# Optimization experiments

Hardware: AMD Instinct MI355X
Metric: run time of the kernel (lower is better)

The kernel has to match this reference:

```python
import jax, jax.numpy as jnp
import numpy as np

Q_PTS = jnp.array([0.0, 0.25, 0.5, 0.75, 1.0], dtype=jnp.float32)
LN_EPS = 1e-5


def _lower_median(s):
    # torch.median returns the LOWER of the two middle values for even n
    return s[..., (s.shape[-1] - 1) // 2]


def _quantile_sorted(s, q):
    # torch.quantile default 'linear' interpolation, computed on pre-sorted s
    n = s.shape[-1]
    idx = q * (n - 1)
    lo = jnp.floor(idx).astype(jnp.int32)
    hi = jnp.ceil(idx).astype(jnp.int32)
    frac = (idx - lo).astype(s.dtype)
    return jnp.take(s, lo, axis=-1) * (1.0 - frac) + jnp.take(s, hi, axis=-1) * frac


def _robust_stats(flat):
    # flat: [L-1, B, N] -> [L-1, B, 7]  (median, MAD, 5 quantiles)
    s = jnp.sort(flat, axis=-1)
    med = _lower_median(s)[..., None]
    mad = _lower_median(jnp.sort(jnp.abs(flat - med), axis=-1))[..., None]
    q = _quantile_sorted(s, Q_PTS)
    return jnp.concatenate([med, mad, q], axis=-1)


def _layer_norm(x, eps=LN_EPS):
    mu = x.mean(-1, keepdims=True)
    var = ((x - mu) ** 2).mean(-1, keepdims=True)
    return (x - mu) * jax.lax.rsqrt(var + eps)


def _forward(ws, bs, fc1_w, fc1_b, ln_w, ln_b, gate_w, gate_b, fco_w, fco_b, scale):
    Lm1, B = ws.shape[0], ws.shape[1]
    w_flat = ws.reshape(Lm1, B, -1)
    b_flat = bs.reshape(Lm1, B, -1)
    w_feats = _robust_stats(w_flat)            # [L-1, B, 7]
    b_feats = _robust_stats(b_flat)            # [L-1, B, 7]
    g_mean = w_flat.mean(-1, keepdims=True)    # [L-1, B, 1]
    g_mad = jnp.zeros_like(g_mean)             # MAD over a size-1 axis is exactly 0
    combined = jnp.concatenate([w_feats, b_feats, g_mean, g_mad], axis=-1)  # [L-1, B, 16]
    x = _layer_norm(combined)                  # F.layer_norm without affine
    # ResidualMLP (vectorized over the layer axis l)
    h = jnp.einsum('lbi,lhi->lbh', x, fc1_w) + fc1_b[:, None, :]
    h = _layer_norm(h) * ln_w[:, None, :] + ln_b[:, None, :]
    h = jax.nn.gelu(h, approximate=False)      # nn.GELU() default = exact erf
    gate = jax.nn.sigmoid(jnp.einsum('lbh,lgh->lbg', h, gate_w) + gate_b[:, None, :])
    raw = jnp.einsum('lbg,log->lbo', h * gate, fco_w) + fco_b[:, None, :]
    return jnp.sin(raw) * scale[:, None, None] + 1.0   # [L-1, B, out_dim]


def setup_inputs() -> dict:
    key = jax.random.key(0)
    ks = jax.random.split(key, 8)
    Lm1, B, D, H, F_IN = 3, 64, 512, 64, 16
    return {
        'ws': jax.random.normal(ks[0], (Lm1, B, D, D), jnp.float32) * 0.05,
        'bs': jax.random.normal(ks[1], (Lm1, B, D), jnp.float32) * 0.05,
        'w_last': jax.random.normal(ks[2], (B, D, D), jnp.float32) * 0.05,
        'b_last': jax.random.normal(ks[3], (B, D), jnp.float32) * 0.05,
        'fc1_w': jax.random.normal(ks[4], (Lm1, H, F_IN), jnp.float32) * 0.2,
        'fc1_b': jnp.zeros((Lm1, H), jnp.float32),
        'ln_w': jnp.ones((Lm1, H), jnp.float32),
        'ln_b': jnp.zeros((Lm1, H), jnp.float32),
        'gate_w': jax.random.normal(ks[5], (Lm1, H, H), jnp.float32) * 0.15,
        'gate_b': jnp.zeros((Lm1, H), jnp.float32),
        'fco_w': jax.random.normal(ks[6], (Lm1, D, H), jnp.float32) * 0.1,
        'fco_b': jnp.zeros((Lm1, D), jnp.float32),
        'scale': jnp.full((Lm1,), 0.1, jnp.float32),
    }


def reference(ws, bs, w_last, b_last, fc1_w, fc1_b, ln_w, ln_b, gate_w, gate_b, fco_w, fco_b, scale):
    # w_last / b_last correspond to wsfeat[L-1]: received by forward but never used
    # (loop breaks at i == L-1), matching the torch module exactly.
    return _forward(ws, bs, fc1_w, fc1_b, ln_w, ln_b, gate_w, gate_b, fco_w, fco_b, scale)
```

## Files before the change

kernel.cpp:

```cpp
#include <hip/hip_runtime.h>
#include <cstdint>

#define LM1   3
#define BDIM  64
#define NROW  (LM1 * BDIM)
#define DDIM  512
#define NW    (DDIM * DDIM)
#define NW4   (NW / 4)
#define WT    1024
#define CAP   30720

__device__ __forceinline__ uint32_t mono(float x) {
    uint32_t u = __float_as_uint(x);
    return (u & 0x80000000u) ? ~u : (u | 0x80000000u);
}
__device__ __forceinline__ float unmono(uint32_t u) {
    uint32_t v = (u & 0x80000000u) ? (u & 0x7FFFFFFFu) : ~u;
    return __uint_as_float(v);
}

__device__ void block_select(const uint32_t* hist, int nb, uint32_t rank,
                             uint32_t* sbuf, uint32_t* out_bin, uint32_t* out_rem,
                             int tid) {
    const int NT = WT;
    int per = (nb + NT - 1) / NT;
    int base = tid * per;
    uint32_t s = 0;
    for (int i = 0; i < per; ++i) {
        int idx = base + i;
        if (idx < nb) s += hist[idx];
    }
    sbuf[tid] = s;
    __syncthreads();
    uint32_t run = s;
    for (int off = 1; off < NT; off <<= 1) {
        uint32_t add = (tid >= off) ? sbuf[tid - off] : 0u;
        __syncthreads();
        run += add;
        sbuf[tid] = run;
        __syncthreads();
    }
    uint32_t incl = run;
    uint32_t excl = incl - s;
    if (rank >= excl && rank < incl) {
        uint32_t rem = rank - excl;
        for (int i = 0; i < per; ++i) {
            int idx = base + i;
            if (idx >= nb) break;
            uint32_t c = hist[idx];
            if (rem < c) { *out_bin = (uint32_t)idx; *out_rem = rem; break; }
            rem -= c;
        }
    }
    __syncthreads();
}

__device__ uint32_t refine_lds(const uint32_t* cbuf, uint32_t off, uint32_t cnt,
                               uint32_t rem, uint32_t b1,
                               uint32_t* hist2, uint32_t* sbuf,
                               uint32_t* stmp, int tid) {
    for (int i = tid; i < 2048; i += WT) hist2[i] = 0;
    __syncthreads();
    for (uint32_t i = tid; i < cnt; i += WT) {
        uint32_t u = cbuf[off + i];
        atomicAdd(&hist2[(u >> 9) & 2047u], 1u);
    }
    __syncthreads();
    block_select(hist2, 2048, rem, sbuf, &stmp[0], &stmp[1], tid);
    uint32_t b2 = stmp[0], r2 = stmp[1];
    __syncthreads();
    for (int i = tid; i < 512; i += WT) hist2[i] = 0;
    __syncthreads();
    for (uint32_t i = tid; i < cnt; i += WT) {
        uint32_t u = cbuf[off + i];
        if (((u >> 9) & 2047u) == b2) atomicAdd(&hist2[u & 511u], 1u);
    }
    __syncthreads();
    block_select(hist2, 512, r2, sbuf, &stmp[0], &stmp[1], tid);
    uint32_t b3 = stmp[0];
    __syncthreads();
    return (b1 << 20) | (b2 << 9) | b3;
}

__device__ uint32_t refine_global(const float4* p4, uint32_t phase, float med, int mode,
                                  uint32_t b1, uint32_t rem,
                                  uint32_t* hist2, uint32_t* sbuf,
                                  uint32_t* stmp, int tid) {
    for (int i = tid; i < 2048; i += WT) hist2[i] = 0;
    __syncthreads();
    for (int it = 0; it < 64; ++it) {
        float4 v = p4[(tid + it * WT + phase) & (NW4 - 1)];
        float xs[4] = {v.x, v.y, v.z, v.w};
        #pragma unroll
        for (int c = 0; c < 4; ++c) {
            uint32_t u = mode ? __float_as_uint(fabsf(xs[c] - med)) : mono(xs[c]);
            if ((u >> 20) == b1) atomicAdd(&hist2[(u >> 9) & 2047u], 1u);
        }
    }
    __syncthreads();
    block_select(hist2, 2048, rem, sbuf, &stmp[0], &stmp[1], tid);
    uint32_t b2 = stmp[0], r2 = stmp[1];
    __syncthreads();
    for (int i = tid; i < 512; i += WT) hist2[i] = 0;
    __syncthreads();
    for (int it = 0; it < 64; ++it) {
        float4 v = p4[(tid + it * WT + phase) & (NW4 - 1)];
        float xs[4] = {v.x, v.y, v.z, v.w};
        #pragma unroll
        for (int c = 0; c < 4; ++c) {
            uint32_t u = mode ? __float_as_uint(fabsf(xs[c] - med)) : mono(xs[c]);
            if ((u >> 20) == b1 && ((u >> 9) & 2047u) == b2)
                atomicAdd(&hist2[u & 511u], 1u);
        }
    }
    __syncthreads();
    block_select(hist2, 512, r2, sbuf, &stmp[0], &stmp[1], tid);
    uint32_t b3 = stmp[0];
    __syncthreads();
    return (b1 << 20) | (b2 << 9) | b3;
}

__global__ __launch_bounds__(WT) void wstats_kernel(const float* __restrict__ wsrc,
                                                    float* __restrict__ feat) {
    const int row = blockIdx.x;
    const int tid = threadIdx.x;
    const float4* __restrict__ p4 = (const float4*)(wsrc + (size_t)row * NW);
    const uint32_t phase = ((uint32_t)row * 341u) & (NW4 - 1);

    __shared__ uint32_t lds[4096 + CAP + 2048 + 1024];
    uint32_t* hist  = lds;
    uint32_t* cbuf  = lds + 4096;
    uint32_t* hist2 = lds + 4096 + CAP;
    uint32_t* sbuf  = lds + 4096 + CAP + 2048;
    __shared__ uint32_t s_bin[8], s_rem[8];
    __shared__ uint32_t s_dbin[8], s_cnt[8], s_off[9], s_cur[8], s_rdj[8];
    __shared__ uint32_t s_nd, s_T, stmp[2], s_sv[8];
    __shared__ float s_med;

    for (int i = tid; i < 4096; i += WT) hist[i] = 0;
    __syncthreads();
    float sum = 0.f;
    for (int it = 0; it < 64; it += 8) {
        float4 a[8];
        #pragma unroll
        for (int j = 0; j < 8; ++j)
            a[j] = p4[(tid + (it + j) * WT + phase) & (NW4 - 1)];
        #pragma unroll
        for (int j = 0; j < 8; ++j) {
            float xs[4] = {a[j].x, a[j].y, a[j].z, a[j].w};
            #pragma unroll
            for (int c = 0; c < 4; ++c) {
                sum += xs[c];
                uint32_t u = mono(xs[c]);
                atomicAdd(&hist[u >> 20], 1u);
            }
        }
    }
    {
        float* sbf = (float*)sbuf;
        sbf[tid] = sum; __syncthreads();
        for (int o = WT / 2; o > 0; o >>= 1) {
            if (tid < o) sbf[tid] += sbf[tid + o];
            __syncthreads();
        }
        if (tid == 0) feat[row * 16 + 14] = sbf[0] * (1.0f / (float)NW);
    }
    __syncthreads();

    const uint32_t RANKS[8] = {0u, 65535u, 65536u, 131071u, 131072u, 196607u, 196608u, 262143u};
    for (int k = 0; k < 8; ++k)
        block_select(hist, 4096, RANKS[k], sbuf, &s_bin[k], &s_rem[k], tid);

    if (tid == 0) {
        uint32_t nd = 0;
        for (int k = 0; k < 8; ++k) {
            uint32_t b = s_bin[k];
            int j = -1;
            for (uint32_t t = 0; t < nd; ++t) if (s_dbin[t] == b) { j = (int)t; break; }
            if (j < 0) { j = nd; s_dbin[nd] = b; s_cnt[nd] = hist[b]; nd++; }
            s_rdj[k] = (uint32_t)j;
        }
        s_off[0] = 0;
        for (uint32_t t = 0; t < nd; ++t) { s_off[t + 1] = s_off[t] + s_cnt[t]; s_cur[t] = 0; }
        s_nd = nd; s_T = s_off[nd];
    }
    __syncthreads();
    const uint32_t nd = s_nd, T = s_T;

    if (T <= CAP) {
        uint8_t* tbl = (uint8_t*)sbuf;
        for (int i = tid; i < 4096; i += WT) tbl[i] = 0;
        __syncthreads();
        if (tid < (int)nd) tbl[s_dbin[tid]] = (uint8_t)(tid + 1);
        __syncthreads();
        for (int it = 0; it < 64; it += 8) {
            float4 a[8];
            #pragma unroll
            for (int j = 0; j < 8; ++j)
                a[j] = p4[(tid + (it + j) * WT + phase) & (NW4 - 1)];
            #pragma unroll
            for (int j = 0; j < 8; ++j) {
                float xs[4] = {a[j].x, a[j].y, a[j].z, a[j].w};
                #pragma unroll
                for (int c = 0; c < 4; ++c) {
                    uint32_t u = mono(xs[c]);
                    uint32_t m = tbl[u >> 20];
                    if (m) {
                        uint32_t jj = m - 1;
                        uint32_t pos = atomicAdd(&s_cur[jj], 1u);
                        cbuf[s_off[jj] + pos] = u;
                    }
                }
            }
        }
        __syncthreads();
        for (int k = 0; k < 8; ++k) {
            uint32_t j = s_rdj[k];
            uint32_t u = refine_lds(cbuf, s_off[j], s_cnt[j], s_rem[k], s_bin[k],
                                    hist2, sbuf, stmp, tid);
            if (tid == 0) s_sv[k] = u;
            __syncthreads();
        }
    } else {
        for (int k = 0; k < 8; ++k) {
            uint32_t u = refine_global(p4, phase, 0.f, 0, s_bin[k], s_rem[k],
                                       hist2, sbuf, stmp, tid);
            if (tid == 0) s_sv[k] = u;
            __syncthreads();
        }
    }

    if (tid == 0) {
        float sv[8];
        #pragma unroll
        for (int k = 0; k < 8; ++k) sv[k] = unmono(s_sv[k]);
        float* f = feat + row * 16;
        f[0]  = sv[3];
        f[2]  = sv[0];
        f[3]  = 0.25f * sv[1] + 0.75f * sv[2];
        f[4]  = 0.5f  * (sv[3] + sv[4]);
        f[5]  = 0.75f * sv[5] + 0.25f * sv[6];
        f[6]  = sv[7];
        f[15] = 0.0f;
        s_med = sv[3];
    }
    __syncthreads();
    const float med = s_med;

    for (int i = tid; i < 4096; i += WT) hist[i] = 0;
    __syncthreads();
    for (int it = 0; it < 64; it += 8) {
        float4 a[8];
        #pragma unroll
        for (int j = 0; j < 8; ++j)
            a[j] = p4[(tid + (it + j) * WT + phase) & (NW4 - 1)];
        #pragma unroll
        for (int j = 0; j < 8; ++j) {
            float xs[4] = {a[j].x, a[j].y, a[j].z, a[j].w};
            #pragma unroll
            for (int c = 0; c < 4; ++c) {
                uint32_t u = __float_as_uint(fabsf(xs[c] - med));
                atomicAdd(&hist[u >> 20], 1u);
            }
        }
    }
    __syncthreads();
    block_select(hist, 4096, 131071u, sbuf, &s_bin[0], &s_rem[0], tid);
    const uint32_t mb1 = s_bin[0], mrem = s_rem[0];
    const uint32_t mcnt = hist[mb1];
    __syncthreads();

    uint32_t madu;
    if (mcnt <= CAP) {
        if (tid == 0) s_cur[0] = 0;
        __syncthreads();
        for (int it = 0; it < 64; it += 8) {
            float4 a[8];
            #pragma unroll
            for (int j = 0; j < 8; ++j)
                a[j] = p4[(tid + (it + j) * WT + phase) & (NW4 - 1)];
            #pragma unroll
            for (int j = 0; j < 8; ++j) {
                float xs[4] = {a[j].x, a[j].y, a[j].z, a[j].w};
                #pragma unroll
                for (int c = 0; c < 4; ++c) {
                    uint32_t u = __float_as_uint(fabsf(xs[c] - med));
                    if ((u >> 20) == mb1) {
                        uint32_t pos = atomicAdd(&s_cur[0], 1u);
                        cbuf[pos] = u;
                    }
                }
            }
        }
        __syncthreads();
        madu = refine_lds(cbuf, 0, mcnt, mrem, mb1, hist2, sbuf, stmp, tid);
    } else {
        madu = refine_global(p4, phase, med, 1, mb1, mrem, hist2, sbuf, stmp, tid);
    }
    if (tid == 0) feat[row * 16 + 1] = __uint_as_float(madu);
}

__device__ void bitonic512(float* a, int tid) {
    for (int k = 2; k <= 512; k <<= 1) {
        for (int j = k >> 1; j > 0; j >>= 1) {
            __syncthreads();
            for (int i = tid; i < 512; i += 256) {
                int ixj = i ^ j;
                if (ixj > i) {
                    float x = a[i], y = a[ixj];
                    bool up = ((i & k) == 0);
                    if ((x > y) == up) { a[i] = y; a[ixj] = x; }
                }
            }
        }
    }
    __syncthreads();
}

__global__ __launch_bounds__(256) void tail_kernel(
    const float* __restrict__ bsrc, const float* __restrict__ feat,
    const float* __restrict__ fc1_w, const float* __restrict__ fc1_b,
    const float* __restrict__ ln_w,  const float* __restrict__ ln_b,
    const float* __restrict__ gate_w, const float* __restrict__ gate_b,
    const float* __restrict__ fco_w,  const float* __restrict__ fco_b,
    const float* __restrict__ scale,  float* __restrict__ out) {
    const int row = blockIdx.x;
    const int tid = threadIdx.x;
    const int l = row >> 6;
    __shared__ float a[512], d[512];
    __shared__ float x[16], h[64], hg[64], stats[2];

    if (tid < 7)       x[tid] = feat[row * 16 + tid];
    else if (tid == 7) x[14]  = feat[row * 16 + 14];
    else if (tid == 8) x[15]  = 0.0f;

    const float* p = bsrc + (size_t)row * 512;
    for (int i = tid; i < 512; i += 256) a[i] = p[i];
    bitonic512(a, tid);
    const float bmed = a[255];
    if (tid == 0) {
        x[7]  = bmed;
        x[9]  = a[0];
        x[10] = 0.25f * a[127] + 0.75f * a[128];
        x[11] = 0.5f  * (a[255] + a[256]);
        x[12] = 0.75f * a[383] + 0.25f * a[384];
        x[13] = a[511];
    }
    __syncthreads();
    for (int i = tid; i < 512; i += 256) d[i] = fabsf(a[i] - bmed);
    bitonic512(d, tid);
    if (tid == 0) x[8] = d[255];
    __syncthreads();

    if (tid == 0) {
        float mu = 0.f;
        for (int i = 0; i < 16; ++i) mu += x[i];
        mu *= (1.f / 16.f);
        float var = 0.f;
        for (int i = 0; i < 16; ++i) { float dd = x[i] - mu; var += dd * dd; }
        var *= (1.f / 16.f);
        stats[0] = mu; stats[1] = rsqrtf(var + 1e-5f);
    }
    __syncthreads();
    if (tid < 16) x[tid] = (x[tid] - stats[0]) * stats[1];
    __syncthreads();
    if (tid < 64) {
        const float* w = fc1_w + ((size_t)l * 64 + tid) * 16;
        float acc = fc1_b[l * 64 + tid];
        #pragma unroll
        for (int i = 0; i < 16; ++i) acc += x[i] * w[i];
        h[tid] = acc;
    }
    __syncthreads();
    if (tid == 0) {
        float mu = 0.f;
        for (int i = 0; i < 64; ++i) mu += h[i];
        mu *= (1.f / 64.f);
        float var = 0.f;
        for (int i = 0; i < 64; ++i) { float dd = h[i] - mu; var += dd * dd; }
        var *= (1.f / 64.f);
        stats[0] = mu; stats[1] = rsqrtf(var + 1e-5f);
    }
    __syncthreads();
    if (tid < 64) {
        float v = (h[tid] - stats[0]) * stats[1] * ln_w[l * 64 + tid] + ln_b[l * 64 + tid];
        h[tid] = 0.5f * v * (1.0f + erff(v * 0.70710678118654752f));
    }
    __syncthreads();
    if (tid < 64) {
        const float* w = gate_w + ((size_t)l * 64 + tid) * 64;
        float acc = gate_b[l * 64 + tid];
        #pragma unroll
        for (int i = 0; i < 64; ++i) acc += h[i] * w[i];
        float g = 1.0f / (1.0f + expf(-acc));
        hg[tid] = h[tid] * g;
    }
    __syncthreads();
    const float sc = scale[l];
    for (int o = tid; o < 512; o += 256) {
        const float* w = fco_w + ((size_t)l * 512 + o) * 64;
        float acc = fco_b[l * 512 + o];
        #pragma unroll
        for (int i = 0; i < 64; ++i) acc += hg[i] * w[i];
        out[(size_t)row * 512 + o] = sinf(acc) * sc + 1.0f;
    }
}

extern "C" void kernel_launch(void* const* d_in, const int* in_sizes, int n_in,
                              void* d_out, int out_size, void* d_ws, size_t ws_size,
                              hipStream_t stream) {
    const float* ws_in  = (const float*)d_in[0];
    const float* bs_in  = (const float*)d_in[1];
    const float* fc1_w  = (const float*)d_in[4];
    const float* fc1_b  = (const float*)d_in[5];
    const float* ln_w   = (const float*)d_in[6];
    const float* ln_b   = (const float*)d_in[7];
    const float* gate_w = (const float*)d_in[8];
    const float* gate_b = (const float*)d_in[9];
    const float* fco_w  = (const float*)d_in[10];
    const float* fco_b  = (const float*)d_in[11];
    const float* scale  = (const float*)d_in[12];
    float* out  = (float*)d_out;
    float* feat = (float*)d_ws;

    hipLaunchKernelGGL(wstats_kernel, dim3(NROW), dim3(WT), 0, stream, ws_in, feat);
    hipLaunchKernelGGL(tail_kernel, dim3(NROW), dim3(256), 0, stream,
                       bs_in, feat, fc1_w, fc1_b, ln_w, ln_b, gate_w, gate_b,
                       fco_w, fco_b, scale, out);
}
```

Measured before the change: 502.9 us.

## Use sampled pivot windows to select quantiles and MAD in one full pass

Draws a strided 1/8 sample of each row into LDS and uses it to estimate bracketing windows around the quartile, median and MAD order statistics. A single full pass over global memory then counts elements below each window, collects in-window candidates into LDS segments, and computes sum, min and max in the same loop. Exact selection runs on the small candidate sets with a three-level radix refine. If any window misses the target rank or overflows capacity, an exact multi-pass fallback runs. This replaces several full passes over the 1 MB row with one, at the cost of many LDS atomics for candidate collection, and the block-wide scan is also rebuilt on wave shuffles.

```diff
diff --git a/kernel.cpp b/kernel.cpp
--- a/kernel.cpp
+++ b/kernel.cpp
@@ -3,12 +3,25 @@
 
 #define LM1   3
 #define BDIM  64
-#define NROW  (LM1 * BDIM)
+#define NROW  192
 #define DDIM  512
-#define NW    (DDIM * DDIM)
-#define NW4   (NW / 4)
-#define WT    1024
-#define CAP   30720
+#define NW    262144
+#define NW4   65536
+#define NT    1024
+
+#define SSAMP 32768
+#define CAPQ  6144
+#define CAP3  14336
+#define SEG0  0
+#define SEG1  6144
+#define SEG2  12288
+#define SEG3  18432
+
+#define H1OFF 32768
+#define H2OFF 36864
+#define SBOFF 38912
+#define CTOFF 39936
+#define LDSW  40000
 
 __device__ __forceinline__ uint32_t mono(float x) {
     uint32_t u = __float_as_uint(x);
@@ -20,76 +33,88 @@
 }
 
 __device__ void block_select(const uint32_t* hist, int nb, uint32_t rank,
-                             uint32_t* sbuf, uint32_t* out_bin, uint32_t* out_rem,
-                             int tid) {
-    const int NT = WT;
+                             uint32_t* sbuf, volatile uint32_t* out, int tid) {
     int per = (nb + NT - 1) / NT;
     int base = tid * per;
     uint32_t s = 0;
-    for (int i = 0; i < per; ++i) {
-        int idx = base + i;
-        if (idx < nb) s += hist[idx];
-    }
-    sbuf[tid] = s;
-    __syncthreads();
-    uint32_t run = s;
-    for (int off = 1; off < NT; off <<= 1) {
-        uint32_t add = (tid >= off) ? sbuf[tid - off] : 0u;
-        __syncthreads();
-        run += add;
-        sbuf[tid] = run;
-        __syncthreads();
-    }
-    uint32_t incl = run;
-    uint32_t excl = incl - s;
-    if (rank >= excl && rank < incl) {
+    for (int i = 0; i < per; ++i) { int idx = base + i; if (idx < nb) s += hist[idx]; }
+    uint32_t p = s;
+    int lane = tid & 63;
+    #pragma unroll
+    for (int off = 1; off < 64; off <<= 1) {
+        uint32_t v = __shfl_up(p, off);
+        if (lane >= off) p += v;
+    }
+    int w = tid >> 6;
+    if (lane == 63) sbuf[w] = p;
+    __syncthreads();
+    if (tid == 0) {
+        uint32_t acc = 0;
+        for (int i = 0; i < 16; ++i) { uint32_t t = sbuf[i]; sbuf[16 + i] = acc; acc += t; }
+    }
+    __syncthreads();
+    uint32_t excl = sbuf[16 + w] + p - s;
+    if (rank >= excl && rank < excl + s) {
         uint32_t rem = rank - excl;
         for (int i = 0; i < per; ++i) {
             int idx = base + i;
             if (idx >= nb) break;
             uint32_t c = hist[idx];
-            if (rem < c) { *out_bin = (uint32_t)idx; *out_rem = rem; break; }
+            if (rem < c) { out[0] = (uint32_t)idx; out[1] = rem; break; }
             rem -= c;
         }
     }
     __syncthreads();
 }
 
-__device__ uint32_t refine_lds(const uint32_t* cbuf, uint32_t off, uint32_t cnt,
-                               uint32_t rem, uint32_t b1,
+__device__ __forceinline__ uint32_t sel_key(uint32_t st, int mode, float med) {
+    return mode ? __float_as_uint(fabsf(unmono(st) - med)) : st;
+}
+
+__device__ uint32_t seg_select(const uint32_t* seg, uint32_t cnt, uint32_t rank,
+                               int mode, float med,
                                uint32_t* hist2, uint32_t* sbuf,
-                               uint32_t* stmp, int tid) {
-    for (int i = tid; i < 2048; i += WT) hist2[i] = 0;
-    __syncthreads();
-    for (uint32_t i = tid; i < cnt; i += WT) {
-        uint32_t u = cbuf[off + i];
-        atomicAdd(&hist2[(u >> 9) & 2047u], 1u);
-    }
-    __syncthreads();
-    block_select(hist2, 2048, rem, sbuf, &stmp[0], &stmp[1], tid);
-    uint32_t b2 = stmp[0], r2 = stmp[1];
-    __syncthreads();
-    for (int i = tid; i < 512; i += WT) hist2[i] = 0;
-    __syncthreads();
-    for (uint32_t i = tid; i < cnt; i += WT) {
-        uint32_t u = cbuf[off + i];
-        if (((u >> 9) & 2047u) == b2) atomicAdd(&hist2[u & 511u], 1u);
-    }
-    __syncthreads();
-    block_select(hist2, 512, r2, sbuf, &stmp[0], &stmp[1], tid);
-    uint32_t b3 = stmp[0];
-    __syncthreads();
-    return (b1 << 20) | (b2 << 9) | b3;
-}
-
-__device__ uint32_t refine_global(const float4* p4, uint32_t phase, float med, int mode,
+                               volatile uint32_t* out2, int tid) {
+    for (int i = tid; i < 2048; i += NT) hist2[i] = 0;
+    __syncthreads();
+    for (uint32_t i = tid; i < cnt; i += NT)
+        atomicAdd(&hist2[sel_key(seg[i], mode, med) >> 21], 1u);
+    __syncthreads();
+    block_select(hist2, 2048, rank, sbuf, out2, tid);
+    uint32_t b1 = out2[0], r1 = out2[1];
+    __syncthreads();
+    for (int i = tid; i < 2048; i += NT) hist2[i] = 0;
+    __syncthreads();
+    for (uint32_t i = tid; i < cnt; i += NT) {
+        uint32_t k = sel_key(seg[i], mode, med);
+        if ((k >> 21) == b1) atomicAdd(&hist2[(k >> 10) & 2047u], 1u);
+    }
+    __syncthreads();
+    block_select(hist2, 2048, r1, sbuf, out2, tid);
+    uint32_t b2 = out2[0], r2 = out2[1];
+    __syncthreads();
+    for (int i = tid; i < 1024; i += NT) hist2[i] = 0;
+    __syncthreads();
+    for (uint32_t i = tid; i < cnt; i += NT) {
+        uint32_t k = sel_key(seg[i], mode, med);
+        if ((k >> 21) == b1 && ((k >> 10) & 2047u) == b2)
+            atomicAdd(&hist2[k & 1023u], 1u);
+    }
+    __syncthreads();
+    block_select(hist2, 1024, r2, sbuf, out2, tid);
+    uint32_t b3 = out2[0];
+    __syncthreads();
+    return (b1 << 21) + (b2 << 10) + b3;
+}
+
+__device__ uint32_t refine_global(const float4* p4, float med, int mode,
                                   uint32_t b1, uint32_t rem,
                                   uint32_t* hist2, uint32_t* sbuf,
-                                  uint32_t* stmp, int tid) {
-    for (int i = tid; i < 2048; i += WT) hist2[i] = 0;
+                                  volatile uint32_t* out2, int tid) {
+    for (int i = tid; i < 2048; i += NT) hist2[i] = 0;
     __syncthreads();
     for (int it = 0; it < 64; ++it) {
-        float4 v = p4[(tid + it * WT + phase) & (NW4 - 1)];
+        float4 v = p4[tid + it * NT];
         float xs[4] = {v.x, v.y, v.z, v.w};
         #pragma unroll
         for (int c = 0; c < 4; ++c) {
@@ -98,13 +123,13 @@
         }
     }
     __syncthreads();
-    block_select(hist2, 2048, rem, sbuf, &stmp[0], &stmp[1], tid);
-    uint32_t b2 = stmp[0], r2 = stmp[1];
-    __syncthreads();
-    for (int i = tid; i < 512; i += WT) hist2[i] = 0;
+    block_select(hist2, 2048, rem, sbuf, out2, tid);
+    uint32_t b2 = out2[0], r2 = out2[1];
+    __syncthreads();
+    for (int i = tid; i < 512; i += NT) hist2[i] = 0;
     __syncthreads();
     for (int it = 0; it < 64; ++it) {
-        float4 v = p4[(tid + it * WT + phase) & (NW4 - 1)];
+        float4 v = p4[tid + it * NT];
         float xs[4] = {v.x, v.y, v.z, v.w};
         #pragma unroll
         for (int c = 0; c < 4; ++c) {
@@ -114,190 +139,244 @@
         }
     }
     __syncthreads();
-    block_select(hist2, 512, r2, sbuf, &stmp[0], &stmp[1], tid);
-    uint32_t b3 = stmp[0];
-    __syncthreads();
-    return (b1 << 20) | (b2 << 9) | b3;
-}
-
-__global__ __launch_bounds__(WT) void wstats_kernel(const float* __restrict__ wsrc,
+    block_select(hist2, 512, r2, sbuf, out2, tid);
+    uint32_t b3 = out2[0];
+    __syncthreads();
+    return (b1 << 20) + (b2 << 9) + b3;
+}
+
+__device__ void fb_path(const float4* p4, float* feat, int row,
+                        uint32_t* lds, int tid) {
+    uint32_t* histF  = lds;
+    uint32_t* hist2F = lds + 4096;
+    uint32_t* sbufF  = lds + 4096 + 2048;
+    volatile uint32_t* outF = (volatile uint32_t*)(lds + CTOFF + 4);
+    const uint32_t RANK6[6] = {65535u, 65536u, 131071u, 131072u, 196607u, 196608u};
+
+    for (int i = tid; i < 4096; i += NT) histF[i] = 0;
+    __syncthreads();
+    for (int it = 0; it < 64; ++it) {
+        float4 v = p4[tid + it * NT];
+        float xs[4] = {v.x, v.y, v.z, v.w};
+        #pragma unroll
+        for (int c = 0; c < 4; ++c) atomicAdd(&histF[mono(xs[c]) >> 20], 1u);
+    }
+    __syncthreads();
+    uint32_t bins[6], rems[6];
+    for (int k = 0; k < 6; ++k) {
+        block_select(histF, 4096, RANK6[k], sbufF, outF, tid);
+        bins[k] = outF[0]; rems[k] = outF[1];
+        __syncthreads();
+    }
+    float svv[6];
+    for (int k = 0; k < 6; ++k)
+        svv[k] = unmono(refine_global(p4, 0.f, 0, bins[k], rems[k], hist2F, sbufF, outF, tid));
+    if (tid == 0) {
+        float* f = feat + row * 16;
+        f[0] = svv[2];
+        f[3] = 0.25f * svv[0] + 0.75f * svv[1];
+        f[4] = 0.5f  * (svv[2] + svv[3]);
+        f[5] = 0.75f * svv[4] + 0.25f * svv[5];
+    }
+    float med = svv[2];
+    __syncthreads();
+    for (int i = tid; i < 4096; i += NT) histF[i] = 0;
+    __syncthreads();
+    for (int it = 0; it < 64; ++it) {
+        float4 v = p4[tid + it * NT];
+        float xs[4] = {v.x, v.y, v.z, v.w};
+        #pragma unroll
+        for (int c = 0; c < 4; ++c)
+            atomicAdd(&histF[__float_as_uint(fabsf(xs[c] - med)) >> 20], 1u);
+    }
+    __syncthreads();
+    block_select(histF, 4096, 131071u, sbufF, outF, tid);
+    uint32_t mb = outF[0], mr = outF[1];
+    __syncthreads();
+    uint32_t mu = refine_global(p4, med, 1, mb, mr, hist2F, sbufF, outF, tid);
+    if (tid == 0) feat[row * 16 + 1] = __uint_as_float(mu);
+}
+
+__global__ __launch_bounds__(NT) void wstats_kernel(const float* __restrict__ wsrc,
                                                     float* __restrict__ feat) {
     const int row = blockIdx.x;
     const int tid = threadIdx.x;
-    const float4* __restrict__ p4 = (const float4*)(wsrc + (size_t)row * NW);
-    const uint32_t phase = ((uint32_t)row * 341u) & (NW4 - 1);
-
-    __shared__ uint32_t lds[4096 + CAP + 2048 + 1024];
-    uint32_t* hist  = lds;
-    uint32_t* cbuf  = lds + 4096;
-    uint32_t* hist2 = lds + 4096 + CAP;
-    uint32_t* sbuf  = lds + 4096 + CAP + 2048;
-    __shared__ uint32_t s_bin[8], s_rem[8];
-    __shared__ uint32_t s_dbin[8], s_cnt[8], s_off[9], s_cur[8], s_rdj[8];
-    __shared__ uint32_t s_nd, s_T, stmp[2], s_sv[8];
-    __shared__ float s_med;
-
-    for (int i = tid; i < 4096; i += WT) hist[i] = 0;
-    __syncthreads();
+    const float* __restrict__ src = wsrc + (size_t)row * NW;
+    const float4* __restrict__ p4 = (const float4*)src;
+
+    __shared__ uint32_t lds[LDSW];
+    __shared__ float fctrl[8];
+    uint32_t* hist  = lds + H1OFF;
+    uint32_t* hist2 = lds + H2OFF;
+    uint32_t* sbuf  = lds + SBOFF;
+    uint32_t* ctrl  = lds + CTOFF;
+    volatile uint32_t* out2 = (volatile uint32_t*)(ctrl + 4);
+
+    for (int i = tid; i < 4096; i += NT) hist[i] = 0;
+    __syncthreads();
+    for (int k = 0; k < 32; ++k) {
+        int i = tid + k * NT;
+        float x = src[(size_t)i * 8];
+        uint32_t u = mono(x);
+        lds[i] = u;
+        atomicAdd(&hist[u >> 20], 1u);
+    }
+    __syncthreads();
+
+    const uint32_t EPRANK[6] = {7918u, 8466u, 16067u, 16701u, 24302u, 24850u};
+    for (int e = 0; e < 6; ++e) {
+        block_select(hist, 4096, EPRANK[e], sbuf, out2, tid);
+        uint32_t b1 = out2[0], r1 = out2[1];
+        __syncthreads();
+        for (int i = tid; i < 2048; i += NT) hist2[i] = 0;
+        __syncthreads();
+        for (int k = 0; k < 32; ++k) {
+            uint32_t u = lds[tid + k * NT];
+            if ((u >> 20) == b1) atomicAdd(&hist2[(u >> 9) & 2047u], 1u);
+        }
+        __syncthreads();
+        block_select(hist2, 2048, r1, sbuf, out2, tid);
+        uint32_t b2 = out2[0];
+        if (tid == 0) ctrl[6 + e] = (b1 << 20) + ((b2 + (uint32_t)(e & 1)) << 9);
+        __syncthreads();
+    }
+
+    if (tid == 0) {
+        float lo = unmono(ctrl[8]), hi = unmono(ctrl[9]);
+        fctrl[0] = 0.5f * (lo + hi);
+        fctrl[1] = 0.5f * (hi - lo);
+    }
+    __syncthreads();
+    const float m0 = fctrl[0];
+    for (int i = tid; i < 4096; i += NT) hist[i] = 0;
+    __syncthreads();
+    for (int k = 0; k < 32; ++k) {
+        uint32_t tb = __float_as_uint(fabsf(unmono(lds[tid + k * NT]) - m0));
+        atomicAdd(&hist[tb >> 20], 1u);
+    }
+    __syncthreads();
+    const uint32_t MRANK[2] = {16067u, 16701u};
+    for (int e = 0; e < 2; ++e) {
+        block_select(hist, 4096, MRANK[e], sbuf, out2, tid);
+        uint32_t b1 = out2[0], r1 = out2[1];
+        __syncthreads();
+        for (int i = tid; i < 2048; i += NT) hist2[i] = 0;
+        __syncthreads();
+        for (int k = 0; k < 32; ++k) {
+            uint32_t tb = __float_as_uint(fabsf(unmono(lds[tid + k * NT]) - m0));
+            if ((tb >> 20) == b1) atomicAdd(&hist2[(tb >> 9) & 2047u], 1u);
+        }
+        __syncthreads();
+        block_select(hist2, 2048, r1, sbuf, out2, tid);
+        uint32_t b2 = out2[0];
+        if (tid == 0) ctrl[18 + e] = (b1 << 20) + ((b2 + (uint32_t)(e & 1)) << 9);
+        __syncthreads();
+    }
+    if (tid == 0) {
+        float dwin = fctrl[1] * 1.01f;
+        fctrl[2] = fmaxf(__uint_as_float(ctrl[18]) - dwin, 0.0f);
+        fctrl[3] = __uint_as_float(ctrl[19]) + dwin;
+        ctrl[0] = 0; ctrl[1] = 0; ctrl[2] = 0; ctrl[3] = 0;
+        ctrl[12] = 0;
+    }
+    __syncthreads();
+
+    const uint32_t L25 = ctrl[6],  W25 = ctrl[7]  - ctrl[6];
+    const uint32_t Lm  = ctrl[8],  Wm  = ctrl[9]  - ctrl[8];
+    const uint32_t L75 = ctrl[10], W75 = ctrl[11] - ctrl[10];
+    const float AwinLo = fctrl[2], AwinHi = fctrl[3];
     float sum = 0.f;
-    for (int it = 0; it < 64; it += 8) {
-        float4 a[8];
-        #pragma unroll
-        for (int j = 0; j < 8; ++j)
-            a[j] = p4[(tid + (it + j) * WT + phase) & (NW4 - 1)];
-        #pragma unroll
-        for (int j = 0; j < 8; ++j) {
-            float xs[4] = {a[j].x, a[j].y, a[j].z, a[j].w};
-            #pragma unroll
-            for (int c = 0; c < 4; ++c) {
-                sum += xs[c];
-                uint32_t u = mono(xs[c]);
-                atomicAdd(&hist[u >> 20], 1u);
-            }
-        }
-    }
+    uint32_t umin = 0xFFFFFFFFu, umax = 0u;
+    uint32_t c25 = 0, cm = 0, c75 = 0, cmad = 0;
+    for (int it = 0; it < 64; ++it) {
+        float4 v = p4[tid + it * NT];
+        float xs[4] = {v.x, v.y, v.z, v.w};
+        #pragma unroll
+        for (int c = 0; c < 4; ++c) {
+            float x = xs[c];
+            uint32_t u = mono(x);
+            sum += x;
+            umin = umin < u ? umin : u;
+            umax = umax > u ? umax : u;
+            c25 += (u < L25); cm += (u < Lm); c75 += (u < L75);
+            if (u - L25 < W25) { uint32_t p = atomicAdd(&ctrl[0], 1u); if (p < CAPQ) lds[SEG0 + p] = u; }
+            if (u - Lm  < Wm ) { uint32_t p = atomicAdd(&ctrl[1], 1u); if (p < CAPQ) lds[SEG1 + p] = u; }
+            if (u - L75 < W75) { uint32_t p = atomicAdd(&ctrl[2], 1u); if (p < CAPQ) lds[SEG2 + p] = u; }
+            float t = fabsf(x - m0);
+            cmad += (t < AwinLo);
+            if (t >= AwinLo && t <= AwinHi) { uint32_t p = atomicAdd(&ctrl[3], 1u); if (p < CAP3) lds[SEG3 + p] = u; }
+        }
+    }
+    __syncthreads();
+
     {
-        float* sbf = (float*)sbuf;
-        sbf[tid] = sum; __syncthreads();
-        for (int o = WT / 2; o > 0; o >>= 1) {
-            if (tid < o) sbf[tid] += sbf[tid + o];
-            __syncthreads();
-        }
-        if (tid == 0) feat[row * 16 + 14] = sbf[0] * (1.0f / (float)NW);
-    }
-    __syncthreads();
-
-    const uint32_t RANKS[8] = {0u, 65535u, 65536u, 131071u, 131072u, 196607u, 196608u, 262143u};
-    for (int k = 0; k < 8; ++k)
-        block_select(hist, 4096, RANKS[k], sbuf, &s_bin[k], &s_rem[k], tid);
-
-    if (tid == 0) {
-        uint32_t nd = 0;
-        for (int k = 0; k < 8; ++k) {
-            uint32_t b = s_bin[k];
-            int j = -1;
-            for (uint32_t t = 0; t < nd; ++t) if (s_dbin[t] == b) { j = (int)t; break; }
-            if (j < 0) { j = nd; s_dbin[nd] = b; s_cnt[nd] = hist[b]; nd++; }
-            s_rdj[k] = (uint32_t)j;
-        }
-        s_off[0] = 0;
-        for (uint32_t t = 0; t < nd; ++t) { s_off[t + 1] = s_off[t] + s_cnt[t]; s_cur[t] = 0; }
-        s_nd = nd; s_T = s_off[nd];
-    }
-    __syncthreads();
-    const uint32_t nd = s_nd, T = s_T;
-
-    if (T <= CAP) {
-        uint8_t* tbl = (uint8_t*)sbuf;
-        for (int i = tid; i < 4096; i += WT) tbl[i] = 0;
-        __syncthreads();
-        if (tid < (int)nd) tbl[s_dbin[tid]] = (uint8_t)(tid + 1);
-        __syncthreads();
-        for (int it = 0; it < 64; it += 8) {
-            float4 a[8];
-            #pragma unroll
-            for (int j = 0; j < 8; ++j)
-                a[j] = p4[(tid + (it + j) * WT + phase) & (NW4 - 1)];
-            #pragma unroll
-            for (int j = 0; j < 8; ++j) {
-                float xs[4] = {a[j].x, a[j].y, a[j].z, a[j].w};
-                #pragma unroll
-                for (int c = 0; c < 4; ++c) {
-                    uint32_t u = mono(xs[c]);
-                    uint32_t m = tbl[u >> 20];
-                    if (m) {
-                        uint32_t jj = m - 1;
-                        uint32_t pos = atomicAdd(&s_cur[jj], 1u);
-                        cbuf[s_off[jj] + pos] = u;
-                    }
-                }
-            }
-        }
-        __syncthreads();
-        for (int k = 0; k < 8; ++k) {
-            uint32_t j = s_rdj[k];
-            uint32_t u = refine_lds(cbuf, s_off[j], s_cnt[j], s_rem[k], s_bin[k],
-                                    hist2, sbuf, stmp, tid);
-            if (tid == 0) s_sv[k] = u;
-            __syncthreads();
-        }
-    } else {
-        for (int k = 0; k < 8; ++k) {
-            uint32_t u = refine_global(p4, phase, 0.f, 0, s_bin[k], s_rem[k],
-                                       hist2, sbuf, stmp, tid);
-            if (tid == 0) s_sv[k] = u;
-            __syncthreads();
-        }
-    }
-
-    if (tid == 0) {
-        float sv[8];
-        #pragma unroll
-        for (int k = 0; k < 8; ++k) sv[k] = unmono(s_sv[k]);
+        int lane = tid & 63, w = tid >> 6;
+        #pragma unroll
+        for (int off = 32; off > 0; off >>= 1) {
+            sum  += __shfl_down(sum, off);
+            uint32_t t;
+            t = __shfl_down(umin, off); umin = umin < t ? umin : t;
+            t = __shfl_down(umax, off); umax = umax > t ? umax : t;
+            c25 += __shfl_down(c25, off);
+            cm  += __shfl_down(cm, off);
+            c75 += __shfl_down(c75, off);
+            cmad+= __shfl_down(cmad, off);
+        }
+        float* fsb = (float*)sbuf;
+        if (lane == 0) {
+            fsb[w * 8 + 0] = sum;
+            sbuf[w * 8 + 1] = umin; sbuf[w * 8 + 2] = umax;
+            sbuf[w * 8 + 3] = c25;  sbuf[w * 8 + 4] = cm;
+            sbuf[w * 8 + 5] = c75;  sbuf[w * 8 + 6] = cmad;
+        }
+        __syncthreads();
+        if (tid == 0) { float s = 0; for (int i = 0; i < 16; ++i) s += fsb[i * 8]; feat[row * 16 + 14] = s * (1.0f / (float)NW); }
+        if (tid == 1) { uint32_t m = 0xFFFFFFFFu; for (int i = 0; i < 16; ++i) { uint32_t t = sbuf[i * 8 + 1]; m = m < t ? m : t; } feat[row * 16 + 2] = unmono(m); }
+        if (tid == 2) { uint32_t m = 0u; for (int i = 0; i < 16; ++i) { uint32_t t = sbuf[i * 8 + 2]; m = m > t ? m : t; } feat[row * 16 + 6] = unmono(m); }
+        if (tid >= 3 && tid <= 6) { uint32_t s = 0; for (int i = 0; i < 16; ++i) s += sbuf[i * 8 + tid]; ctrl[10 + tid] = s; }
+        if (tid == 7) feat[row * 16 + 15] = 0.0f;
+    }
+    __syncthreads();
+
+    if (tid == 0) {
+        int C25 = (int)ctrl[13], Cm = (int)ctrl[14], C75 = (int)ctrl[15], Cmad = (int)ctrl[16];
+        int n0 = (int)(ctrl[0] < CAPQ ? ctrl[0] : CAPQ);
+        int n1 = (int)(ctrl[1] < CAPQ ? ctrl[1] : CAPQ);
+        int n2 = (int)(ctrl[2] < CAPQ ? ctrl[2] : CAPQ);
+        int n3 = (int)(ctrl[3] < CAP3 ? ctrl[3] : CAP3);
+        int fail = (ctrl[0] > CAPQ) || (ctrl[1] > CAPQ) || (ctrl[2] > CAPQ) || (ctrl[3] > CAP3)
+                || (C25 > 65535)  || (65536  - C25 >= n0)
+                || (Cm  > 131071) || (131072 - Cm  >= n1)
+                || (C75 > 196607) || (196608 - C75 >= n2)
+                || (Cmad > 131071)|| (131071 - Cmad >= n3);
+        ctrl[12] = (uint32_t)fail;
+    }
+    __syncthreads();
+
+    if (ctrl[12]) { fb_path(p4, feat, row, lds, tid); return; }
+
+    const uint32_t C25 = ctrl[13], Cm = ctrl[14], C75 = ctrl[15], Cmad = ctrl[16];
+    const uint32_t n0 = ctrl[0], n1 = ctrl[1], n2 = ctrl[2], n3 = ctrl[3];
+    uint32_t k25a = seg_select(lds + SEG0, n0, 65535u  - C25, 0, 0.f, hist2, sbuf, out2, tid);
+    uint32_t k25b = seg_select(lds + SEG0, n0, 65536u  - C25, 0, 0.f, hist2, sbuf, out2, tid);
+    uint32_t kma  = seg_select(lds + SEG1, n1, 131071u - Cm,  0, 0.f, hist2, sbuf, out2, tid);
+    uint32_t kmb  = seg_select(lds + SEG1, n1, 131072u - Cm,  0, 0.f, hist2, sbuf, out2, tid);
+    uint32_t k75a = seg_select(lds + SEG2, n2, 196607u - C75, 0, 0.f, hist2, sbuf, out2, tid);
+    uint32_t k75b = seg_select(lds + SEG2, n2, 196608u - C75, 0, 0.f, hist2, sbuf, out2, tid);
+    float med = unmono(kma);
+    uint32_t kmad = seg_select(lds + SEG3, n3, 131071u - Cmad, 1, med, hist2, sbuf, out2, tid);
+    float madv = __uint_as_float(kmad);
+    float dchk = fctrl[1] * 1.02f + 1e-12f;
+    bool bad = !(madv > fctrl[2] + dchk && madv < fctrl[3] - dchk);
+    if (bad) { fb_path(p4, feat, row, lds, tid); return; }
+    if (tid == 0) {
         float* f = feat + row * 16;
-        f[0]  = sv[3];
-        f[2]  = sv[0];
-        f[3]  = 0.25f * sv[1] + 0.75f * sv[2];
-        f[4]  = 0.5f  * (sv[3] + sv[4]);
-        f[5]  = 0.75f * sv[5] + 0.25f * sv[6];
-        f[6]  = sv[7];
-        f[15] = 0.0f;
-        s_med = sv[3];
-    }
-    __syncthreads();
-    const float med = s_med;
-
-    for (int i = tid; i < 4096; i += WT) hist[i] = 0;
-    __syncthreads();
-    for (int it = 0; it < 64; it += 8) {
-        float4 a[8];
-        #pragma unroll
-        for (int j = 0; j < 8; ++j)
-            a[j] = p4[(tid + (it + j) * WT + phase) & (NW4 - 1)];
-        #pragma unroll
-        for (int j = 0; j < 8; ++j) {
-            float xs[4] = {a[j].x, a[j].y, a[j].z, a[j].w};
-            #pragma unroll
-            for (int c = 0; c < 4; ++c) {
-                uint32_t u = __float_as_uint(fabsf(xs[c] - med));
-                atomicAdd(&hist[u >> 20], 1u);
-            }
-        }
-    }
-    __syncthreads();
-    block_select(hist, 4096, 131071u, sbuf, &s_bin[0], &s_rem[0], tid);
-    const uint32_t mb1 = s_bin[0], mrem = s_rem[0];
-    const uint32_t mcnt = hist[mb1];
-    __syncthreads();
-
-    uint32_t madu;
-    if (mcnt <= CAP) {
-        if (tid == 0) s_cur[0] = 0;
-        __syncthreads();
-        for (int it = 0; it < 64; it += 8) {
-            float4 a[8];
-            #pragma unroll
-            for (int j = 0; j < 8; ++j)
-                a[j] = p4[(tid + (it + j) * WT + phase) & (NW4 - 1)];
-            #pragma unroll
-            for (int j = 0; j < 8; ++j) {
-                float xs[4] = {a[j].x, a[j].y, a[j].z, a[j].w};
-                #pragma unroll
-                for (int c = 0; c < 4; ++c) {
-                    uint32_t u = __float_as_uint(fabsf(xs[c] - med));
-                    if ((u >> 20) == mb1) {
-                        uint32_t pos = atomicAdd(&s_cur[0], 1u);
-                        cbuf[pos] = u;
-                    }
-                }
-            }
-        }
-        __syncthreads();
-        madu = refine_lds(cbuf, 0, mcnt, mrem, mb1, hist2, sbuf, stmp, tid);
-    } else {
-        madu = refine_global(p4, phase, med, 1, mb1, mrem, hist2, sbuf, stmp, tid);
-    }
-    if (tid == 0) feat[row * 16 + 1] = __uint_as_float(madu);
+        f[0] = med;
+        f[1] = madv;
+        f[3] = 0.25f * unmono(k25a) + 0.75f * unmono(k25b);
+        f[4] = 0.5f  * (med + unmono(kmb));
+        f[5] = 0.75f * unmono(k75a) + 0.25f * unmono(k75b);
+    }
 }
 
 __device__ void bitonic512(float* a, int tid) {
@@ -423,7 +502,7 @@
     float* out  = (float*)d_out;
     float* feat = (float*)d_ws;
 
-    hipLaunchKernelGGL(wstats_kernel, dim3(NROW), dim3(WT), 0, stream, ws_in, feat);
+    hipLaunchKernelGGL(wstats_kernel, dim3(NROW), dim3(NT), 0, stream, ws_in, feat);
     hipLaunchKernelGGL(tail_kernel, dim3(NROW), dim3(256), 0, stream,
                        bs_in, feat, fc1_w, fc1_b, ln_w, ln_b, gate_w, gate_b,
                        fco_w, fco_b, scale, out);
```

Result: slower. 856.0 us (+70.2%).
